# Performance work log

Measured on AMD Instinct MI355X. Metric: run time of the kernel, lower is better.

## Reference

```python
import jax, jax.numpy as jnp
import numpy as np

N_NODES = 100000
N_EDGES = 3200000
D_IN = 256
D_OUT = 256


def setup_inputs() -> dict:
    key = jax.random.key(0)
    k1, k2, k3, k4, k5, k6 = jax.random.split(key, 6)
    x = jax.random.normal(k1, (N_NODES, D_IN), dtype=jnp.float32)
    edge_row = jax.random.randint(k2, (N_EDGES,), 0, N_NODES, dtype=jnp.int32)
    edge_col = jax.random.randint(k3, (N_EDGES,), 0, N_NODES, dtype=jnp.int32)
    edge_val = jax.random.uniform(k4, (N_EDGES,), dtype=jnp.float32)
    # nn.Linear params (PyTorch stores weight as [out, in]; we apply x @ W.T + b)
    bound = 1.0 / np.sqrt(D_IN)
    W = jax.random.uniform(k5, (D_OUT, D_IN), minval=-bound, maxval=bound, dtype=jnp.float32)
    b = jax.random.uniform(k6, (D_OUT,), minval=-bound, maxval=bound, dtype=jnp.float32)
    return {"x": x, "edge_row": edge_row, "edge_col": edge_col,
            "edge_val": edge_val, "W": W, "b": b}


def reference(x, edge_row, edge_col, edge_val, W, b):
    # SpMM: agg[i] = sum over edges e with row[e]==i of val[e] * x[col[e]]
    messages = edge_val[:, None] * x[edge_col]          # [E, D_in]
    agg = jax.ops.segment_sum(messages, edge_row, num_segments=N_NODES)  # [N, D_in]
    # Dense linear: agg @ W.T + b
    return jnp.einsum('nd,od->no', agg, W) + b
```

## Files before the change

### kernel.cpp

```cpp
#include <hip/hip_runtime.h>

#define THREADS 256
#define P2T 512

typedef __attribute__((ext_vector_type(8))) short short8;
typedef __attribute__((ext_vector_type(4))) float f32x4;

__device__ __forceinline__ unsigned short f2bf(float f) {
    unsigned u = __builtin_bit_cast(unsigned, f);
    return (unsigned short)((u + 0x7FFFu + ((u >> 16) & 1u)) >> 16);
}
__device__ __forceinline__ float bf2f_lo(unsigned u) { return __builtin_bit_cast(float, u << 16); }
__device__ __forceinline__ float bf2f_hi(unsigned u) { return __builtin_bit_cast(float, u & 0xFFFF0000u); }

#define P1B 1024

__global__ void fusedA_kernel(const int* __restrict__ row, const int* __restrict__ col,
                              const float* __restrict__ val, int* __restrict__ gcur,
                              uint2* __restrict__ estage,
                              const float* __restrict__ W, unsigned short* __restrict__ WbP,
                              const float4* __restrict__ x, uint4* __restrict__ xb,
                              int n_edges, int nbkt, int capB, int n8) {
    int b = blockIdx.x, tid = threadIdx.x;
    if (b < P1B) {
        __shared__ int h[512];
        __shared__ int curl[512];
        int E0 = (int)((long long)b * n_edges / P1B);
        int E1 = (int)((long long)(b + 1) * n_edges / P1B);
        for (int i = tid; i < 512; i += THREADS) h[i] = 0;
        __syncthreads();
        for (int e = E0 + tid; e < E1; e += THREADS)
            atomicAdd(&h[row[e] >> 8], 1);
        __syncthreads();
        for (int bk = tid; bk < nbkt; bk += THREADS) {
            int c = h[bk];
            curl[bk] = bk * capB + (c ? atomicAdd(&gcur[bk], c) : 0);
        }
        __syncthreads();
        for (int e = E0 + tid; e < E1; e += THREADS) {
            int r = row[e];
            int bk = r >> 8;
            int pos = atomicAdd(&curl[bk], 1);
            if (pos < (bk + 1) * capB)
                estage[pos] = make_uint2(((unsigned)(r & 255) << 24) | (unsigned)col[e],
                                         (unsigned)__float_as_int(val[e]));
        }
    } else if (b < P1B + 32) {
        int f = (b - P1B) * THREADS + tid;
        int l = f & 63, nt = (f >> 6) & 15, k0i = f >> 10;
        int r = nt * 16 + (l & 15);
        int koff = k0i * 32 + 8 * (l >> 4);
        const float4* s = reinterpret_cast<const float4*>(W + r * 256 + koff);
        float4 a = s[0], bb = s[1];
        uint4 o;
        o.x = (unsigned)f2bf(a.x) | ((unsigned)f2bf(a.y) << 16);
        o.y = (unsigned)f2bf(a.z) | ((unsigned)f2bf(a.w) << 16);
        o.z = (unsigned)f2bf(bb.x) | ((unsigned)f2bf(bb.y) << 16);
        o.w = (unsigned)f2bf(bb.z) | ((unsigned)f2bf(bb.w) << 16);
        reinterpret_cast<uint4*>(WbP)[f] = o;
    } else {
        int i = (b - P1B - 32) * THREADS + tid;
        if (i >= n8) return;
        float4 a = x[2 * i], bb = x[2 * i + 1];
        uint4 o;
        o.x = (unsigned)f2bf(a.x) | ((unsigned)f2bf(a.y) << 16);
        o.y = (unsigned)f2bf(a.z) | ((unsigned)f2bf(a.w) << 16);
        o.z = (unsigned)f2bf(bb.x) | ((unsigned)f2bf(bb.y) << 16);
        o.w = (unsigned)f2bf(bb.z) | ((unsigned)f2bf(bb.w) << 16);
        reinterpret_cast<uint4*>(xb)[i] = o;
    }
}

__global__ void p2_sort(const uint2* __restrict__ estage, const int* __restrict__ gcur,
                        int2* __restrict__ pr, int* __restrict__ offs,
                        int capB, int n_nodes, int nbkt) {
    __shared__ int red[P2T];
    __shared__ int h[256];
    __shared__ int curh[256];
    __shared__ int wsum[4];
    int b = blockIdx.x, tid = threadIdx.x;

    int partial = 0;
    for (int j = tid; j < b; j += P2T) {
        int c = gcur[j];
        partial += c > capB ? capB : c;
    }
    red[tid] = partial;
    __syncthreads();
    #pragma unroll
    for (int s = P2T / 2; s > 0; s >>= 1) {
        if (tid < s) red[tid] += red[tid + s];
        __syncthreads();
    }
    int gb = red[0];
    int count = gcur[b]; if (count > capB) count = capB;
    int base = b * capB;

    if (tid < 256) h[tid] = 0;
    __syncthreads();
    for (int i = tid; i < count; i += P2T)
        atomicAdd(&h[estage[base + i].x >> 24], 1);
    __syncthreads();
    if (tid < 256) {
        int v = h[tid];
        int lane = tid & 63, w = tid >> 6;
        int incl = v;
        #pragma unroll
        for (int off = 1; off < 64; off <<= 1) {
            int t = __shfl_up(incl, off, 64);
            if (lane >= off) incl += t;
        }
        if (lane == 63) wsum[w] = incl;
        __syncthreads();
        int wo = 0;
        for (int i = 0; i < w; ++i) wo += wsum[i];
        int excl = wo + incl - v;
        int node = b * 256 + tid;
        if (node < n_nodes) offs[node] = gb + excl;
        curh[tid] = gb + excl;
    } else {
        __syncthreads();
    }
    if (b == nbkt - 1 && tid == 0) offs[n_nodes] = gb + count;
    __syncthreads();
    for (int i = tid; i < count; i += P2T) {
        uint2 p = estage[base + i];
        int q = atomicAdd(&curh[(int)(p.x >> 24)], 1);
        pr[q] = make_int2((int)(p.x & 0x00FFFFFFu), (int)p.y);
    }
}

template<int OUT_BF16>
__global__ void spmm_bf16_kernel(const uint2* __restrict__ xb, const int* __restrict__ offs,
                                 const int2* __restrict__ pr, void* __restrict__ outp,
                                 int b0, int b1, int nnodes) {
    int g = blockIdx.x & 7;
    int inst = blockIdx.x >> 3;
    int bkt = b0 + g + 8 * (inst >> 6);
    if (bkt >= b1) return;
    int wid = bkt * 256 + (inst & 63) * 4 + (threadIdx.x >> 6);
    int lane = threadIdx.x & 63;
    if (wid >= nnodes) return;
    int s = offs[wid], e = offs[wid + 1];
    float a0 = 0.f, a1 = 0.f, a2 = 0.f, a3 = 0.f;
    int i = s;
    if (i < e && (i & 1)) {
        int2 p = pr[i];
        uint2 xv = xb[(size_t)p.x * 64 + lane];
        float v = __int_as_float(p.y);
        a0 = fmaf(v, bf2f_lo(xv.x), a0); a1 = fmaf(v, bf2f_hi(xv.x), a1);
        a2 = fmaf(v, bf2f_lo(xv.y), a2); a3 = fmaf(v, bf2f_hi(xv.y), a3);
        ++i;
    }
    for (; i + 8 <= e; i += 8) {
        int4 pa = *reinterpret_cast<const int4*>(pr + i);
        int4 pb = *reinterpret_cast<const int4*>(pr + i + 2);
        int4 pc = *reinterpret_cast<const int4*>(pr + i + 4);
        int4 pd = *reinterpret_cast<const int4*>(pr + i + 6);
        uint2 x0 = xb[(size_t)pa.x * 64 + lane];
        uint2 x1 = xb[(size_t)pa.z * 64 + lane];
        uint2 x2 = xb[(size_t)pb.x * 64 + lane];
        uint2 x3 = xb[(size_t)pb.z * 64 + lane];
        uint2 x4_ = xb[(size_t)pc.x * 64 + lane];
        uint2 x5 = xb[(size_t)pc.z * 64 + lane];
        uint2 x6 = xb[(size_t)pd.x * 64 + lane];
        uint2 x7 = xb[(size_t)pd.z * 64 + lane];
        float v0 = __int_as_float(pa.y), v1 = __int_as_float(pa.w);
        float v2 = __int_as_float(pb.y), v3 = __int_as_float(pb.w);
        float v4 = __int_as_float(pc.y), v5 = __int_as_float(pc.w);
        float v6 = __int_as_float(pd.y), v7 = __int_as_float(pd.w);
        a0 = fmaf(v0, bf2f_lo(x0.x), a0); a1 = fmaf(v0, bf2f_hi(x0.x), a1);
        a2 = fmaf(v0, bf2f_lo(x0.y), a2); a3 = fmaf(v0, bf2f_hi(x0.y), a3);
        a0 = fmaf(v1, bf2f_lo(x1.x), a0); a1 = fmaf(v1, bf2f_hi(x1.x), a1);
        a2 = fmaf(v1, bf2f_lo(x1.y), a2); a3 = fmaf(v1, bf2f_hi(x1.y), a3);
        a0 = fmaf(v2, bf2f_lo(x2.x), a0); a1 = fmaf(v2, bf2f_hi(x2.x), a1);
        a2 = fmaf(v2, bf2f_lo(x2.y), a2); a3 = fmaf(v2, bf2f_hi(x2.y), a3);
        a0 = fmaf(v3, bf2f_lo(x3.x), a0); a1 = fmaf(v3, bf2f_hi(x3.x), a1);
        a2 = fmaf(v3, bf2f_lo(x3.y), a2); a3 = fmaf(v3, bf2f_hi(x3.y), a3);
        a0 = fmaf(v4, bf2f_lo(x4_.x), a0); a1 = fmaf(v4, bf2f_hi(x4_.x), a1);
        a2 = fmaf(v4, bf2f_lo(x4_.y), a2); a3 = fmaf(v4, bf2f_hi(x4_.y), a3);
        a0 = fmaf(v5, bf2f_lo(x5.x), a0); a1 = fmaf(v5, bf2f_hi(x5.x), a1);
        a2 = fmaf(v5, bf2f_lo(x5.y), a2); a3 = fmaf(v5, bf2f_hi(x5.y), a3);
        a0 = fmaf(v6, bf2f_lo(x6.x), a0); a1 = fmaf(v6, bf2f_hi(x6.x), a1);
        a2 = fmaf(v6, bf2f_lo(x6.y), a2); a3 = fmaf(v6, bf2f_hi(x6.y), a3);
        a0 = fmaf(v7, bf2f_lo(x7.x), a0); a1 = fmaf(v7, bf2f_hi(x7.x), a1);
        a2 = fmaf(v7, bf2f_lo(x7.y), a2); a3 = fmaf(v7, bf2f_hi(x7.y), a3);
    }
    for (; i + 2 <= e; i += 2) {
        int4 pa = *reinterpret_cast<const int4*>(pr + i);
        uint2 x0 = xb[(size_t)pa.x * 64 + lane];
        uint2 x1 = xb[(size_t)pa.z * 64 + lane];
        float v0 = __int_as_float(pa.y), v1 = __int_as_float(pa.w);
        a0 = fmaf(v0, bf2f_lo(x0.x), a0); a1 = fmaf(v0, bf2f_hi(x0.x), a1);
        a2 = fmaf(v0, bf2f_lo(x0.y), a2); a3 = fmaf(v0, bf2f_hi(x0.y), a3);
        a0 = fmaf(v1, bf2f_lo(x1.x), a0); a1 = fmaf(v1, bf2f_hi(x1.x), a1);
        a2 = fmaf(v1, bf2f_lo(x1.y), a2); a3 = fmaf(v1, bf2f_hi(x1.y), a3);
    }
    for (; i < e; ++i) {
        int2 p = pr[i];
        uint2 xv = xb[(size_t)p.x * 64 + lane];
        float v = __int_as_float(p.y);
        a0 = fmaf(v, bf2f_lo(xv.x), a0); a1 = fmaf(v, bf2f_hi(xv.x), a1);
        a2 = fmaf(v, bf2f_lo(xv.y), a2); a3 = fmaf(v, bf2f_hi(xv.y), a3);
    }
    if (OUT_BF16) {
        ushort4 o;
        o.x = f2bf(a0); o.y = f2bf(a1); o.z = f2bf(a2); o.w = f2bf(a3);
        *reinterpret_cast<ushort4*>((unsigned short*)outp + (size_t)wid * 256 + 4 * lane) = o;
    } else {
        ((float4*)outp)[(size_t)wid * 64 + lane] = make_float4(a0, a1, a2, a3);
    }
}

__global__ void spmm_f32_kernel(const float4* __restrict__ x4, const int* __restrict__ offs,
                                const int2* __restrict__ pr, float4* __restrict__ out4,
                                int nnodes) {
    int wid = (blockIdx.x * blockDim.x + threadIdx.x) >> 6;
    int lane = threadIdx.x & 63;
    if (wid >= nnodes) return;
    int s = offs[wid], e = offs[wid + 1];
    float4 acc = make_float4(0.f, 0.f, 0.f, 0.f);
    for (int i = s; i < e; ++i) {
        int2 p = pr[i];
        float4 xv = x4[(size_t)p.x * 64 + lane];
        float v = __int_as_float(p.y);
        acc.x = fmaf(v, xv.x, acc.x); acc.y = fmaf(v, xv.y, acc.y);
        acc.z = fmaf(v, xv.z, acc.z); acc.w = fmaf(v, xv.w, acc.w);
    }
    out4[(size_t)wid * 64 + lane] = acc;
}

__launch_bounds__(256)
__global__ void gemm_direct3_kernel(const unsigned short* __restrict__ aggb,
                                    const unsigned short* __restrict__ WbP,
                                    const float* __restrict__ bias,
                                    float* __restrict__ out, int n) {
    int tid = threadIdx.x, lane = tid & 63, w = tid >> 6;
    int row0 = blockIdx.x * 128 + w * 32;
    int lr = lane & 15, lg = lane >> 4;
    const unsigned short* arow0 = aggb + (size_t)(row0 + lr) * 256 + lg * 8;
    const unsigned short* arow1 = arow0 + 16 * 256;
    short8 af0[8], af1[8];
    #pragma unroll
    for (int k = 0; k < 8; ++k) {
        af0[k] = *reinterpret_cast<const short8*>(arow0 + k * 32);
        af1[k] = *reinterpret_cast<const short8*>(arow1 + k * 32);
    }
    #pragma unroll
    for (int half = 0; half < 2; ++half) {
        f32x4 acc0[8], acc1[8];
        #pragma unroll
        for (int nt = 0; nt < 8; ++nt) {
            acc0[nt] = (f32x4){0.f, 0.f, 0.f, 0.f};
            acc1[nt] = (f32x4){0.f, 0.f, 0.f, 0.f};
        }
        #pragma unroll
        for (int k = 0; k < 8; ++k) {
            #pragma unroll
            for (int nt = 0; nt < 8; ++nt) {
                short8 bf_ = *reinterpret_cast<const short8*>(
                    &WbP[(size_t)((k * 16 + half * 8 + nt) * 64 + lane) * 8]);
                acc0[nt] = __builtin_amdgcn_mfma_f32_16x16x32_bf16(af0[k], bf_, acc0[nt], 0, 0, 0);
                acc1[nt] = __builtin_amdgcn_mfma_f32_16x16x32_bf16(af1[k], bf_, acc1[nt], 0, 0, 0);
            }
        }
        #pragma unroll
        for (int nt = 0; nt < 8; ++nt) {
            int gc = half * 128 + nt * 16 + lr;
            float bv = bias[gc];
            #pragma unroll
            for (int q = 0; q < 4; ++q) {
                int gr0 = row0 + lg * 4 + q;
                int gr1 = gr0 + 16;
                if (gr0 < n) out[(size_t)gr0 * 256 + gc] = acc0[nt][q] + bv;
                if (gr1 < n) out[(size_t)gr1 * 256 + gc] = acc1[nt][q] + bv;
            }
        }
    }
}


__global__ void zero_kernel(int* __restrict__ p, int n) {
    int i = blockIdx.x * blockDim.x + threadIdx.x;
    if (i < n) p[i] = 0;
}

__global__ void hist_part_kernel(const int* __restrict__ row, int* __restrict__ cnt,
                                 int n_edges, int n_nodes) {
    int g = blockIdx.x & 7;
    int inst = blockIdx.x >> 3;
    int ninst = gridDim.x >> 3;
    int lo = (int)(((long long)g * n_nodes) >> 3);
    int hi = (int)(((long long)(g + 1) * n_nodes) >> 3);
    int e0 = (int)(((long long)inst * n_edges) / ninst);
    int e1 = (int)(((long long)(inst + 1) * n_edges) / ninst);
    for (int e = e0 + threadIdx.x; e < e1; e += THREADS) {
        int r = row[e];
        if (r >= lo && r < hi) atomicAdd(&cnt[r], 1);
    }
}

__global__ void place_part_kernel(const int* __restrict__ row, const int* __restrict__ col,
                                  const float* __restrict__ val, int* __restrict__ cur,
                                  int2* __restrict__ pr, int n_edges, int n_nodes) {
    int g = blockIdx.x & 7;
    int inst = blockIdx.x >> 3;
    int ninst = gridDim.x >> 3;
    int lo = (int)(((long long)g * n_nodes) >> 3);
    int hi = (int)(((long long)(g + 1) * n_nodes) >> 3);
    int e0 = (int)(((long long)inst * n_edges) / ninst);
    int e1 = (int)(((long long)(inst + 1) * n_edges) / ninst);
    for (int e = e0 + threadIdx.x; e < e1; e += THREADS) {
        int r = row[e];
        if (r >= lo && r < hi) {
            int p = atomicAdd(&cur[r], 1);
            pr[p] = make_int2(col[e], __float_as_int(val[e]));
        }
    }
}

__global__ void scan1_kernel(const int* __restrict__ cnt, int* __restrict__ offs,
                             int* __restrict__ bsum, int n) {
    int tid = threadIdx.x;
    int base = blockIdx.x * 1024 + tid * 4;
    int v0 = 0, v1 = 0, v2 = 0, v3 = 0;
    if (base + 3 < n) {
        int4 v = *reinterpret_cast<const int4*>(cnt + base);
        v0 = v.x; v1 = v.y; v2 = v.z; v3 = v.w;
    } else {
        if (base + 0 < n) v0 = cnt[base + 0];
        if (base + 1 < n) v1 = cnt[base + 1];
        if (base + 2 < n) v2 = cnt[base + 2];
    }
    int ts = v0 + v1 + v2 + v3;
    int lane = tid & 63;
    int incl = ts;
    #pragma unroll
    for (int off = 1; off < 64; off <<= 1) {
        int t = __shfl_up(incl, off, 64);
        if (lane >= off) incl += t;
    }
    __shared__ int wsum[4];
    int w = tid >> 6;
    if (lane == 63) wsum[w] = incl;
    __syncthreads();
    int wo = 0;
    for (int i = 0; i < w; ++i) wo += wsum[i];
    int excl = wo + incl - ts;
    if (base + 0 < n) offs[base + 0] = excl;
    if (base + 1 < n) offs[base + 1] = excl + v0;
    if (base + 2 < n) offs[base + 2] = excl + v0 + v1;
    if (base + 3 < n) offs[base + 3] = excl + v0 + v1 + v2;
    if (tid == THREADS - 1) bsum[blockIdx.x] = wo + incl;
}

__global__ void scan2_kernel(int* __restrict__ bsum, int nb) {
    int tid = threadIdx.x;
    int base = tid * 4;
    int v0 = 0, v1 = 0, v2 = 0, v3 = 0;
    if (base + 0 < nb) v0 = bsum[base + 0];
    if (base + 1 < nb) v1 = bsum[base + 1];
    if (base + 2 < nb) v2 = bsum[base + 2];
    if (base + 3 < nb) v3 = bsum[base + 3];
    int ts = v0 + v1 + v2 + v3;
    int lane = tid & 63;
    int incl = ts;
    #pragma unroll
    for (int off = 1; off < 64; off <<= 1) {
        int t = __shfl_up(incl, off, 64);
        if (lane >= off) incl += t;
    }
    __shared__ int wsum[4];
    int w = tid >> 6;
    if (lane == 63) wsum[w] = incl;
    __syncthreads();
    int wo = 0;
    for (int i = 0; i < w; ++i) wo += wsum[i];
    int excl = wo + incl - ts;
    if (base + 0 < nb) bsum[base + 0] = excl;
    if (base + 1 < nb) bsum[base + 1] = excl + v0;
    if (base + 2 < nb) bsum[base + 2] = excl + v0 + v1;
    if (base + 3 < nb) bsum[base + 3] = excl + v0 + v1 + v2;
    if (tid == THREADS - 1) bsum[nb] = wo + incl;
}

__global__ void scan3_kernel(int* __restrict__ offs, const int* __restrict__ bsum,
                             int* __restrict__ cur, int n) {
    int i = blockIdx.x * blockDim.x + threadIdx.x;
    if (i < n) {
        int v = offs[i] + bsum[i >> 10];
        offs[i] = v;
        cur[i] = v;
    }
    if (i == 0) offs[n] = bsum[(n + 1023) >> 10];
}

__global__ void cvt_bf16_kernel(const float4* __restrict__ in, uint4* __restrict__ out, int n8) {
    int i = blockIdx.x * blockDim.x + threadIdx.x;
    if (i >= n8) return;
    float4 a = in[2 * i], b = in[2 * i + 1];
    uint4 o;
    o.x = (unsigned)f2bf(a.x) | ((unsigned)f2bf(a.y) << 16);
    o.y = (unsigned)f2bf(a.z) | ((unsigned)f2bf(a.w) << 16);
    o.z = (unsigned)f2bf(b.x) | ((unsigned)f2bf(b.y) << 16);
    o.w = (unsigned)f2bf(b.z) | ((unsigned)f2bf(b.w) << 16);
    out[i] = o;
}

__launch_bounds__(256, 2)
__global__ void gemm_mfma_kernel(float* __restrict__ out, const unsigned short* __restrict__ Wb,
                                 const float* __restrict__ bias, int nrows) {
    __shared__ unsigned short As[64][264];
    __shared__ unsigned short Ws[256][40];
    int tid = threadIdx.x;
    int rowBase = blockIdx.x * 64;

    const float4* o4 = reinterpret_cast<const float4*>(out);
    for (int it = tid; it < 64 * 64; it += 256) {
        int r = it >> 6, c = it & 63;
        float4 v = make_float4(0.f, 0.f, 0.f, 0.f);
        int gr = rowBase + r;
        if (gr < nrows) v = o4[(size_t)gr * 64 + c];
        ushort4 w;
        w.x = f2bf(v.x); w.y = f2bf(v.y); w.z = f2bf(v.z); w.w = f2bf(v.w);
        *reinterpret_cast<ushort4*>(&As[r][c * 4]) = w;
    }

    int w = tid >> 6, lane = tid & 63;
    int lr = lane & 15, lg = lane >> 4;
    f32x4 acc[16];
    #pragma unroll
    for (int nt = 0; nt < 16; ++nt) acc[nt] = (f32x4){0.f, 0.f, 0.f, 0.f};

    for (int k0 = 0; k0 < 256; k0 += 32) {
        __syncthreads();
        for (int it = tid; it < 1024; it += 256) {
            int r = it >> 2, c = it & 3;
            uint4 v = *reinterpret_cast<const uint4*>(Wb + (size_t)r * 256 + k0 + c * 8);
            *reinterpret_cast<uint4*>(&Ws[r][c * 8]) = v;
        }
        __syncthreads();
        short8 af = *reinterpret_cast<const short8*>(&As[w * 16 + lr][k0 + 8 * lg]);
        #pragma unroll
        for (int nt = 0; nt < 16; ++nt) {
            short8 bf_ = *reinterpret_cast<const short8*>(&Ws[nt * 16 + lr][8 * lg]);
            acc[nt] = __builtin_amdgcn_mfma_f32_16x16x32_bf16(af, bf_, acc[nt], 0, 0, 0);
        }
    }

    #pragma unroll
    for (int nt = 0; nt < 16; ++nt) {
        int gc = nt * 16 + lr;
        float bv = bias[gc];
        #pragma unroll
        for (int q = 0; q < 4; ++q) {
            int gr = rowBase + w * 16 + lg * 4 + q;
            if (gr < nrows) out[(size_t)gr * 256 + gc] = acc[nt][q] + bv;
        }
    }
}


extern "C" void kernel_launch(void* const* d_in, const int* in_sizes, int n_in,
                              void* d_out, int out_size, void* d_ws, size_t ws_size,
                              hipStream_t stream) {
    const float* x     = (const float*)d_in[0];
    const int*   erow  = (const int*)d_in[1];
    const int*   ecol  = (const int*)d_in[2];
    const float* evalv = (const float*)d_in[3];
    const float* W     = (const float*)d_in[4];
    const float* bias  = (const float*)d_in[5];
    float* out = (float*)d_out;

    int n_nodes = in_sizes[0] / 256;
    int n_edges = in_sizes[1];

    int nbkt = (n_nodes + 255) >> 8;
    int avg = n_edges / (nbkt > 0 ? nbkt : 1);
    int capB = avg + avg / 4 + 1024;

    size_t A = (size_t)((n_nodes + 63) & ~63) + 64;
    int* offs  = (int*)d_ws;
    int* gcur  = offs + A;
    unsigned short* WbP = (unsigned short*)(gcur + 512);
    int2* pr = (int2*)(WbP + 65536);
    int* after_pr = (int*)(pr + n_edges);

    size_t est_ints  = (size_t)nbkt * capB * 2;
    size_t aggb_ints = (size_t)n_nodes * 128 + 32768;
    size_t xb_ints   = (size_t)n_nodes * 128;
    size_t alias_ints = est_ints > aggb_ints ? est_ints : aggb_ints;
    size_t head_ints = (size_t)(after_pr - (int*)d_ws);
    size_t need_new = (head_ints + alias_ints + xb_ints) * 4;
    bool new_ok = (nbkt <= 512) && (nbkt >= 1) && (n_nodes <= (1 << 24)) && ws_size >= need_new;

    if (new_ok) {
        uint2* estage = (uint2*)after_pr;
        unsigned short* aggb = (unsigned short*)after_pr;
        unsigned short* xb = (unsigned short*)(after_pr + alias_ints);

        hipMemsetAsync(gcur, 0, 512 * sizeof(int), stream);
        int n8 = n_nodes * 32;
        int cvtx_blocks = (n8 + THREADS - 1) / THREADS;
        fusedA_kernel<<<P1B + 32 + cvtx_blocks, THREADS, 0, stream>>>(
            erow, ecol, evalv, gcur, estage, W, WbP, (const float4*)x, (uint4*)xb,
            n_edges, nbkt, capB, n8);
        p2_sort<<<nbkt, P2T, 0, stream>>>(estage, gcur, pr, offs, capB, n_nodes, nbkt);

        int b0 = 0;
        for (int sseg = 1; sseg <= 3; ++sseg) {
            int b1 = (sseg == 3) ? nbkt : ((nbkt * sseg / 3) & ~7);
            if (b1 <= b0) continue;
            int grid = 8 * (((b1 - b0) + 7) / 8) * 64;
            spmm_bf16_kernel<1><<<grid, THREADS, 0, stream>>>(
                (const uint2*)xb, offs, pr, aggb, b0, b1, n_nodes);
            b0 = b1;
        }
        int gb = (n_nodes + 127) / 128;
        gemm_direct3_kernel<<<gb, THREADS, 0, stream>>>(aggb, WbP, bias, out, n_nodes);
    } else {
        int nb = (n_nodes + 1023) >> 10;
        size_t Af = (size_t)((n_nodes + 63) & ~63);
        int* cnt   = (int*)d_ws;
        int* offsf = cnt + Af;
        int* cur   = offsf + Af;
        int* bsum  = cur + Af;
        int* wbase = bsum + (((size_t)nb + 64) & ~63ull);
        unsigned short* Wbf = (unsigned short*)wbase;
        int2* prf  = (int2*)(Wbf + 65536);
        int* aft   = (int*)(prf + n_edges);
        unsigned short* xbf = (unsigned short*)aft;
        size_t need_old = (size_t)((char*)(xbf + (size_t)n_nodes * 256) - (char*)d_ws);
        bool told = ws_size >= need_old;

        zero_kernel<<<(n_nodes + THREADS - 1) / THREADS, THREADS, 0, stream>>>(cnt, n_nodes);
        hist_part_kernel<<<2048, THREADS, 0, stream>>>(erow, cnt, n_edges, n_nodes);
        scan1_kernel<<<nb, THREADS, 0, stream>>>(cnt, offsf, bsum, n_nodes);
        scan2_kernel<<<1, THREADS, 0, stream>>>(bsum, nb);
        scan3_kernel<<<(n_nodes + THREADS - 1) / THREADS, THREADS, 0, stream>>>(offsf, bsum, cur, n_nodes);
        place_part_kernel<<<2048, THREADS, 0, stream>>>(erow, ecol, evalv, cur, prf, n_edges, n_nodes);
        cvt_bf16_kernel<<<32, THREADS, 0, stream>>>((const float4*)W, (uint4*)Wbf, 65536 / 8);

        int gb = (n_nodes + 63) / 64;
        if (told) {
            int n8 = n_nodes * 32;
            cvt_bf16_kernel<<<(n8 + THREADS - 1) / THREADS, THREADS, 0, stream>>>(
                (const float4*)x, (uint4*)xbf, n8);
            int nbf = (n_nodes + 255) / 256;
            int gridf = 8 * ((nbf + 7) / 8) * 64;
            spmm_bf16_kernel<0><<<gridf, THREADS, 0, stream>>>(
                (const uint2*)xbf, offsf, prf, out, 0, nbf, n_nodes);
        } else {
            int spmm_blocks_f = (n_nodes + 3) / 4;
            spmm_f32_kernel<<<spmm_blocks_f, THREADS, 0, stream>>>(
                (const float4*)x, offsf, prf, (float4*)out, n_nodes);
        }
        gemm_mfma_kernel<<<gb, THREADS, 0, stream>>>(out, Wbf, bias, n_nodes);
    }
}
```

Measured before the change: 427.8 us.

## Split bucket staging into 8 sub-buckets per bucket to spread global atomics

New measurement: 428.5 us. Within noise of the previous version (+0.2%).

```diff
diff --git a/kernel.cpp b/kernel.cpp
--- a/kernel.cpp
+++ b/kernel.cpp
@@ -20,11 +20,12 @@
                               uint2* __restrict__ estage,
                               const float* __restrict__ W, unsigned short* __restrict__ WbP,
                               const float4* __restrict__ x, uint4* __restrict__ xb,
-                              int n_edges, int nbkt, int capB, int n8) {
+                              int n_edges, int nbkt, int capS, int n8) {
     int b = blockIdx.x, tid = threadIdx.x;
     if (b < P1B) {
         __shared__ int h[512];
         __shared__ int curl[512];
+        int g = b & 7;
         int E0 = (int)((long long)b * n_edges / P1B);
         int E1 = (int)((long long)(b + 1) * n_edges / P1B);
         for (int i = tid; i < 512; i += THREADS) h[i] = 0;
@@ -34,14 +35,14 @@
         __syncthreads();
         for (int bk = tid; bk < nbkt; bk += THREADS) {
             int c = h[bk];
-            curl[bk] = bk * capB + (c ? atomicAdd(&gcur[bk], c) : 0);
+            curl[bk] = (bk * 8 + g) * capS + (c ? atomicAdd(&gcur[bk * 8 + g], c) : 0);
         }
         __syncthreads();
         for (int e = E0 + tid; e < E1; e += THREADS) {
             int r = row[e];
             int bk = r >> 8;
             int pos = atomicAdd(&curl[bk], 1);
-            if (pos < (bk + 1) * capB)
+            if (pos < (bk * 8 + g + 1) * capS)
                 estage[pos] = make_uint2(((unsigned)(r & 255) << 24) | (unsigned)col[e],
                                          (unsigned)__float_as_int(val[e]));
         }
@@ -73,17 +74,19 @@
 
 __global__ void p2_sort(const uint2* __restrict__ estage, const int* __restrict__ gcur,
                         int2* __restrict__ pr, int* __restrict__ offs,
-                        int capB, int n_nodes, int nbkt) {
+                        int capS, int n_nodes, int nbkt) {
     __shared__ int red[P2T];
     __shared__ int h[256];
     __shared__ int curh[256];
     __shared__ int wsum[4];
+    __shared__ int scnt[8];
     int b = blockIdx.x, tid = threadIdx.x;
 
+    int lim = b * 8;
     int partial = 0;
-    for (int j = tid; j < b; j += P2T) {
+    for (int j = tid; j < lim; j += P2T) {
         int c = gcur[j];
-        partial += c > capB ? capB : c;
+        partial += c > capS ? capS : c;
     }
     red[tid] = partial;
     __syncthreads();
@@ -93,13 +96,20 @@
         __syncthreads();
     }
     int gb = red[0];
-    int count = gcur[b]; if (count > capB) count = capB;
-    int base = b * capB;
-
+    if (tid < 8) {
+        int c = gcur[b * 8 + tid];
+        scnt[tid] = c > capS ? capS : c;
+    }
     if (tid < 256) h[tid] = 0;
     __syncthreads();
-    for (int i = tid; i < count; i += P2T)
-        atomicAdd(&h[estage[base + i].x >> 24], 1);
+
+    #pragma unroll
+    for (int g = 0; g < 8; ++g) {
+        int cnt = scnt[g];
+        int base = (b * 8 + g) * capS;
+        for (int i = tid; i < cnt; i += P2T)
+            atomicAdd(&h[estage[base + i].x >> 24], 1);
+    }
     __syncthreads();
     if (tid < 256) {
         int v = h[tid];
@@ -121,12 +131,22 @@
     } else {
         __syncthreads();
     }
-    if (b == nbkt - 1 && tid == 0) offs[n_nodes] = gb + count;
+    if (b == nbkt - 1 && tid == 0) {
+        int t = 0;
+        #pragma unroll
+        for (int g = 0; g < 8; ++g) t += scnt[g];
+        offs[n_nodes] = gb + t;
+    }
     __syncthreads();
-    for (int i = tid; i < count; i += P2T) {
-        uint2 p = estage[base + i];
-        int q = atomicAdd(&curh[(int)(p.x >> 24)], 1);
-        pr[q] = make_int2((int)(p.x & 0x00FFFFFFu), (int)p.y);
+    #pragma unroll
+    for (int g = 0; g < 8; ++g) {
+        int cnt = scnt[g];
+        int base = (b * 8 + g) * capS;
+        for (int i = tid; i < cnt; i += P2T) {
+            uint2 p = estage[base + i];
+            int q = atomicAdd(&curh[(int)(p.x >> 24)], 1);
+            pr[q] = make_int2((int)(p.x & 0x00FFFFFFu), (int)p.y);
+        }
     }
 }
 
@@ -476,17 +496,17 @@
     int n_edges = in_sizes[1];
 
     int nbkt = (n_nodes + 255) >> 8;
-    int avg = n_edges / (nbkt > 0 ? nbkt : 1);
-    int capB = avg + avg / 4 + 1024;
+    int avg8 = n_edges / (8 * (nbkt > 0 ? nbkt : 1)) + 1;
+    int capS = avg8 + avg8 / 8 + 512;
 
     size_t A = (size_t)((n_nodes + 63) & ~63) + 64;
     int* offs  = (int*)d_ws;
     int* gcur  = offs + A;
-    unsigned short* WbP = (unsigned short*)(gcur + 512);
+    unsigned short* WbP = (unsigned short*)(gcur + 4096);
     int2* pr = (int2*)(WbP + 65536);
     int* after_pr = (int*)(pr + n_edges);
 
-    size_t est_ints  = (size_t)nbkt * capB * 2;
+    size_t est_ints  = (size_t)nbkt * 8 * capS * 2;
     size_t aggb_ints = (size_t)n_nodes * 128 + 32768;
     size_t xb_ints   = (size_t)n_nodes * 128;
     size_t alias_ints = est_ints > aggb_ints ? est_ints : aggb_ints;
@@ -499,17 +519,17 @@
         unsigned short* aggb = (unsigned short*)after_pr;
         unsigned short* xb = (unsigned short*)(after_pr + alias_ints);
 
-        hipMemsetAsync(gcur, 0, 512 * sizeof(int), stream);
+        hipMemsetAsync(gcur, 0, 4096 * sizeof(int), stream);
         int n8 = n_nodes * 32;
         int cvtx_blocks = (n8 + THREADS - 1) / THREADS;
         fusedA_kernel<<<P1B + 32 + cvtx_blocks, THREADS, 0, stream>>>(
             erow, ecol, evalv, gcur, estage, W, WbP, (const float4*)x, (uint4*)xb,
-            n_edges, nbkt, capB, n8);
-        p2_sort<<<nbkt, P2T, 0, stream>>>(estage, gcur, pr, offs, capB, n_nodes, nbkt);
+            n_edges, nbkt, capS, n8);
+        p2_sort<<<nbkt, P2T, 0, stream>>>(estage, gcur, pr, offs, capS, n_nodes, nbkt);
 
         int b0 = 0;
-        for (int sseg = 1; sseg <= 3; ++sseg) {
-            int b1 = (sseg == 3) ? nbkt : ((nbkt * sseg / 3) & ~7);
+        for (int sseg = 1; sseg <= 2; ++sseg) {
+            int b1 = (sseg == 2) ? nbkt : ((nbkt / 2) & ~7);
             if (b1 <= b0) continue;
             int grid = 8 * (((b1 - b0) + 7) / 8) * 64;
             spmm_bf16_kernel<1><<<grid, THREADS, 0, stream>>>(
```
